# Kernel optimization log

Hardware: AMD Instinct MI355X
Metric: run time of the kernel (lower is better)

The kernel has to match this reference:

```python
import jax, jax.numpy as jnp
import numpy as np

N_NODES = 100000
N_EDGES = 800000
H_DIM = 128
E_DIM = 32
N_LAYER = 3


def setup_inputs() -> dict:
    key = jax.random.key(0)
    ks = jax.random.split(key, 5)
    x = jax.random.normal(ks[0], (N_NODES, H_DIM), dtype=jnp.float32)
    edge_index = jax.random.randint(ks[1], (2, N_EDGES), 0, N_NODES, dtype=jnp.int64)
    edge_attr = jax.random.normal(ks[2], (N_EDGES, E_DIM), dtype=jnp.float32)
    fan_in = 2 * H_DIM + E_DIM
    # torch Linear weight layout: [out_features, in_features]
    Wm = jax.random.normal(ks[3], (N_LAYER, H_DIM, fan_in), dtype=jnp.float32) / jnp.sqrt(fan_in)
    bm = jax.random.normal(ks[4], (N_LAYER, H_DIM), dtype=jnp.float32) * 0.01
    return {"x": x, "edge_index": edge_index, "edge_attr": edge_attr, "Wm": Wm, "bm": bm}


def reference(x, edge_index, edge_attr, Wm, bm):
    # PyG flow='source_to_target': row 0 = source (j), row 1 = target (i)
    src = edge_index[0]
    dst = edge_index[1]
    n_nodes = x.shape[0]
    n_layer = Wm.shape[0]
    for l in range(n_layer):  # small fixed layer count
        # message: m_ij = Linear(cat[x_j, x_i, edge_attr])
        m = jnp.concatenate([x[src], x[dst], edge_attr], axis=1)  # [E, 2h+e]
        m = jnp.einsum('ef,hf->eh', m, Wm[l]) + bm[l]             # [E, h]
        # aggr='add': scatter-add messages to target nodes
        x = jax.ops.segment_sum(m, dst, num_segments=n_nodes)     # [N, h]
        x = jax.nn.leaky_relu(x, negative_slope=0.01)
    # residual_connection='none' -> no-op; activate_last=True
    x = jax.nn.leaky_relu(x, negative_slope=0.01)
    return x
```

## Files before the change

### kernel.cpp

```cpp
#include <hip/hip_runtime.h>

#define N_NODES 100000
#define NP      100096
#define N_EDGES 800000
#define HD 128
#define ED 32
#define FAN 288
#define NL 3

#define SCHUNK 2048
#define SBLK   ((N_NODES + SCHUNK - 1) / SCHUNK)

typedef short bf16x8 __attribute__((ext_vector_type(8)));
typedef short bf16x4 __attribute__((ext_vector_type(4)));
typedef float f32x4  __attribute__((ext_vector_type(4)));

__device__ inline float b2f(short s) {
    unsigned u = ((unsigned)(unsigned short)s) << 16;
    return __builtin_bit_cast(float, u);
}
__device__ inline short f2b(float f) {
    unsigned u = __builtin_bit_cast(unsigned, f);
    unsigned r = u + 0x7FFFu + ((u >> 16) & 1u);
    return (short)(r >> 16);
}


__global__ void count_kernel(const int* __restrict__ dst, int* __restrict__ deg) {
    int e = blockIdx.x * 256 + threadIdx.x;
    if (e < N_EDGES) atomicAdd(&deg[dst[e]], 1);
}

__global__ void scan_reduce(const int* __restrict__ deg, int* __restrict__ bsum) {
    __shared__ int ws[4];
    const int tid = threadIdx.x;
    int i0 = blockIdx.x * SCHUNK + tid * 8;
    int t = 0;
    #pragma unroll
    for (int j = 0; j < 8; ++j) {
        int i = i0 + j;
        if (i < N_NODES) t += deg[i];
    }
    #pragma unroll
    for (int off = 32; off >= 1; off >>= 1) t += __shfl_down(t, off, 64);
    if ((tid & 63) == 0) ws[tid >> 6] = t;
    __syncthreads();
    if (tid == 0) bsum[blockIdx.x] = ws[0] + ws[1] + ws[2] + ws[3];
}

__global__ void scan_mid(const int* __restrict__ bsum, int* __restrict__ boff,
                         int* __restrict__ ptr) {
    int lane = threadIdx.x;
    int v = (lane < SBLK) ? bsum[lane] : 0;
    int s = v;
    #pragma unroll
    for (int off = 1; off < 64; off <<= 1) {
        int t = __shfl_up(s, off, 64);
        if (lane >= off) s += t;
    }
    if (lane < SBLK) boff[lane] = s - v;
    if (lane == 63) ptr[N_NODES] = s;
}

__global__ void scan_final(const int* __restrict__ deg, const int* __restrict__ boff,
                           int* __restrict__ ptr, int* __restrict__ cursor) {
    __shared__ int wsum[4];
    const int tid = threadIdx.x;
    const int lane = tid & 63, wid = tid >> 6;
    int i0 = blockIdx.x * SCHUNK + tid * 8;
    int v[8]; int tsum = 0;
    #pragma unroll
    for (int j = 0; j < 8; ++j) {
        int i = i0 + j;
        v[j] = (i < N_NODES) ? deg[i] : 0;
        tsum += v[j];
    }
    int s = tsum;
    #pragma unroll
    for (int off = 1; off < 64; off <<= 1) {
        int t = __shfl_up(s, off, 64);
        if (lane >= off) s += t;
    }
    if (lane == 63) wsum[wid] = s;
    __syncthreads();
    int woff = 0;
    #pragma unroll
    for (int w = 0; w < 4; ++w) if (w < wid) woff += wsum[w];
    int excl = boff[blockIdx.x] + woff + (s - tsum);
    #pragma unroll
    for (int j = 0; j < 8; ++j) {
        int i = i0 + j;
        if (i < N_NODES) { ptr[i] = excl; cursor[i] = excl; }
        excl += v[j];
    }
}

__global__ void fill_kernel(const int* __restrict__ src, const int* __restrict__ dst,
                            int* __restrict__ cursor, int2* __restrict__ csr2) {
    int e = blockIdx.x * 256 + threadIdx.x;
    if (e < N_EDGES) {
        int d = dst[e];
        int slot = atomicAdd(&cursor[d], 1);
        csr2[slot] = make_int2(src[e], e);
    }
}

__global__ void permute_eattr(const int2* __restrict__ csr2, const float* __restrict__ eattr,
                              short* __restrict__ ecsr) {
    int idx = blockIdx.x * 256 + threadIdx.x;
    int s = idx >> 3;
    int g = idx & 7;
    if (s >= N_EDGES) return;
    int e = csr2[s].y;
    float4 v = *reinterpret_cast<const float4*>(eattr + (size_t)e * ED + g * 4);
    bf16x4 o;
    o[0] = f2b(v.x); o[1] = f2b(v.y); o[2] = f2b(v.z); o[3] = f2b(v.w);
    *reinterpret_cast<bf16x4*>(ecsr + (size_t)s * ED + g * 4) = o;
}

__global__ void edge_sum(const short* __restrict__ ecsr, const int* __restrict__ ptr,
                         short* __restrict__ agge, float* __restrict__ degf) {
    int node = blockIdx.x * 32 + (threadIdx.x >> 3);
    int g = threadIdx.x & 7;
    if (node >= N_NODES) return;
    int s0 = ptr[node], s1 = ptr[node + 1];
    float a[4] = {};
    for (int s = s0; s < s1; ++s) {
        bf16x4 v = *reinterpret_cast<const bf16x4*>(ecsr + (size_t)s * ED + g * 4);
        #pragma unroll
        for (int j = 0; j < 4; ++j) a[j] += b2f(v[j]);
    }
    bf16x4 o;
    #pragma unroll
    for (int j = 0; j < 4; ++j) o[j] = f2b(a[j]);
    *reinterpret_cast<bf16x4*>(agge + (size_t)node * ED + g * 4) = o;
    if (g == 0) degf[node] = (float)(s1 - s0);
}

__global__ void wconv_kernel(const float* __restrict__ Wm, short* __restrict__ Wb) {
    int idx = blockIdx.x * 256 + threadIdx.x;
    if (idx < NL * HD * FAN) Wb[idx] = f2b(Wm[idx]);
}

__global__ void xconv_kernel(const float* __restrict__ x, const float* __restrict__ degf,
                             short* __restrict__ xb, short* __restrict__ xd) {
    int i4 = blockIdx.x * 256 + threadIdx.x;
    if (i4 >= N_NODES * (HD / 4)) return;
    int row = i4 >> 5;
    float d = degf[row];
    float4 v = reinterpret_cast<const float4*>(x)[i4];
    bf16x4 o, od;
    float vv[4] = {v.x, v.y, v.z, v.w};
    #pragma unroll
    for (int j = 0; j < 4; ++j) {
        short s = f2b(vv[j]);
        o[j] = s;
        od[j] = f2b(b2f(s) * d);
    }
    *reinterpret_cast<bf16x4*>(xb + (size_t)i4 * 4) = o;
    *reinterpret_cast<bf16x4*>(xd + (size_t)i4 * 4) = od;
}

__global__ void aggregate_kernel(const int* __restrict__ ptr, const int2* __restrict__ csr2,
                                 const short* __restrict__ x, short* __restrict__ agg) {
    int node = blockIdx.x * 16 + (threadIdx.x >> 4);
    int g = threadIdx.x & 15;
    if (node >= N_NODES) return;
    int s0 = ptr[node], s1 = ptr[node + 1];
    float acc0[8] = {}, acc1[8] = {};
    int s = s0;
    int i0 = (s < s1) ? csr2[s].x : 0;
    int i1 = (s + 1 < s1) ? csr2[s + 1].x : 0;
    for (; s + 2 <= s1;) {
        bf16x8 v0 = *reinterpret_cast<const bf16x8*>(x + (size_t)i0 * HD + g * 8);
        bf16x8 v1 = *reinterpret_cast<const bf16x8*>(x + (size_t)i1 * HD + g * 8);
        s += 2;
        i0 = (s < s1) ? csr2[s].x : 0;
        i1 = (s + 1 < s1) ? csr2[s + 1].x : 0;
        #pragma unroll
        for (int j = 0; j < 8; ++j) acc0[j] += b2f(v0[j]);
        #pragma unroll
        for (int j = 0; j < 8; ++j) acc1[j] += b2f(v1[j]);
    }
    if (s < s1) {
        bf16x8 v0 = *reinterpret_cast<const bf16x8*>(x + (size_t)i0 * HD + g * 8);
        #pragma unroll
        for (int j = 0; j < 8; ++j) acc0[j] += b2f(v0[j]);
    }
    bf16x8 o;
    #pragma unroll
    for (int j = 0; j < 8; ++j) o[j] = f2b(acc0[j] + acc1[j]);
    *reinterpret_cast<bf16x8*>(agg + (size_t)node * HD + g * 8) = o;
}

__global__ __launch_bounds__(256) void gemm_mfma(
    const short* __restrict__ aggs,
    const short* __restrict__ xdeg,
    const short* __restrict__ agge,
    const float* __restrict__ degf,
    const short* __restrict__ Wb,
    const float* __restrict__ b,
    float* __restrict__ out_f32,
    short* __restrict__ out_x,
    short* __restrict__ out_xd,
    int last)
{
    const int tid = threadIdx.x;
    const int w = tid >> 6, lane = tid & 63;
    const int wy = w >> 1, wx = w & 1;
    const int m0 = blockIdx.x * 128;
    const int l15 = lane & 15, lq = lane >> 4;
    const int kb = lq * 8;
    const size_t arow = (size_t)(m0 + wy * 64 + l15);

    f32x4 acc[4][4];
    #pragma unroll
    for (int i = 0; i < 4; ++i)
        #pragma unroll
        for (int j = 0; j < 4; ++j) acc[i][j] = (f32x4){0.f, 0.f, 0.f, 0.f};

    #pragma unroll
    for (int kt = 0; kt < 9; ++kt) {
        const short* abase;
        int ld, ko;
        if (kt < 4)      { abase = aggs; ld = HD; ko = kt * 32; }
        else if (kt < 8) { abase = xdeg; ld = HD; ko = kt * 32 - 128; }
        else             { abase = agge; ld = ED; ko = 0; }

        bf16x8 a[4], bf[4];
        #pragma unroll
        for (int mf = 0; mf < 4; ++mf)
            a[mf] = *reinterpret_cast<const bf16x8*>(
                abase + (arow + (size_t)mf * 16) * ld + ko + kb);
        #pragma unroll
        for (int nf = 0; nf < 4; ++nf) {
            int c = wx * 64 + nf * 16 + l15;
            bf[nf] = *reinterpret_cast<const bf16x8*>(
                Wb + (size_t)c * FAN + kt * 32 + kb);
        }
        #pragma unroll
        for (int mf = 0; mf < 4; ++mf)
            #pragma unroll
            for (int nf = 0; nf < 4; ++nf)
                acc[mf][nf] = __builtin_amdgcn_mfma_f32_16x16x32_bf16(
                    a[mf], bf[nf], acc[mf][nf], 0, 0, 0);
    }

    #pragma unroll
    for (int mf = 0; mf < 4; ++mf) {
        int r0 = m0 + wy * 64 + mf * 16 + lq * 4;
        float dg[4];
        #pragma unroll
        for (int j = 0; j < 4; ++j)
            dg[j] = (r0 + j < N_NODES) ? degf[r0 + j] : 0.f;
        #pragma unroll
        for (int nf = 0; nf < 4; ++nf) {
            int c = wx * 64 + nf * 16 + l15;
            float bc = b[c];
            #pragma unroll
            for (int j = 0; j < 4; ++j) {
                int row = r0 + j;
                if (row >= N_NODES) continue;
                float v = acc[mf][nf][j] + dg[j] * bc;
                v = (v >= 0.f) ? v : 0.01f * v;
                if (last) {
                    v = (v >= 0.f) ? v : 0.01f * v;
                    out_f32[(size_t)row * HD + c] = v;
                } else {
                    short xb = f2b(v);
                    out_x[(size_t)row * HD + c] = xb;
                    out_xd[(size_t)row * HD + c] = f2b(b2f(xb) * dg[j]);
                }
            }
        }
    }
}

extern "C" void kernel_launch(void* const* d_in, const int* in_sizes, int n_in,
                              void* d_out, int out_size, void* d_ws, size_t ws_size,
                              hipStream_t stream) {
    const float* x_in  = (const float*)d_in[0];
    const int*   ei    = (const int*)d_in[1];
    const float* eattr = (const float*)d_in[2];
    const float* Wm    = (const float*)d_in[3];
    const float* bm    = (const float*)d_in[4];
    float* out = (float*)d_out;

    char* ws = (char*)d_ws;
    size_t off = 0;
    auto alloc = [&](size_t bytes) -> void* {
        void* p = ws + off;
        off = (off + bytes + 255) & ~(size_t)255;
        return p;
    };
    short* x_bf   = (short*)alloc((size_t)NP * HD * 2);
    short* xdeg   = (short*)alloc((size_t)NP * HD * 2);
    short* aggs   = (short*)alloc((size_t)NP * HD * 2);
    short* agge   = (short*)alloc((size_t)NP * ED * 2);
    float* degf   = (float*)alloc((size_t)NP * 4);
    int*   deg    = (int*)alloc((size_t)N_NODES * 4);
    int*   ptr    = (int*)alloc((size_t)(N_NODES + 1) * 4);
    int*   cursor = (int*)alloc((size_t)N_NODES * 4);
    int2*  csr2   = (int2*)alloc((size_t)N_EDGES * 8);
    short* Wb     = (short*)alloc((size_t)NL * HD * FAN * 2);
    int*   bsum   = (int*)alloc((size_t)SBLK * 4);
    int*   boff   = (int*)alloc((size_t)SBLK * 4);

    short* ecsr = x_bf;

    const int* src = ei;
    const int* dst = ei + N_EDGES;

    hipMemsetAsync(deg, 0, (size_t)N_NODES * 4, stream);
    count_kernel<<<(N_EDGES + 255) / 256, 256, 0, stream>>>(dst, deg);
    scan_reduce<<<SBLK, 256, 0, stream>>>(deg, bsum);
    scan_mid<<<1, 64, 0, stream>>>(bsum, boff, ptr);
    scan_final<<<SBLK, 256, 0, stream>>>(deg, boff, ptr, cursor);
    fill_kernel<<<(N_EDGES + 255) / 256, 256, 0, stream>>>(src, dst, cursor, csr2);
    permute_eattr<<<(N_EDGES * 8 + 255) / 256, 256, 0, stream>>>(csr2, eattr, ecsr);
    edge_sum<<<(N_NODES + 31) / 32, 256, 0, stream>>>(ecsr, ptr, agge, degf);
    wconv_kernel<<<(NL * HD * FAN + 255) / 256, 256, 0, stream>>>(Wm, Wb);
    xconv_kernel<<<(N_NODES * (HD / 4) + 255) / 256, 256, 0, stream>>>(x_in, degf, x_bf, xdeg);

    for (int l = 0; l < NL; ++l) {
        aggregate_kernel<<<(N_NODES + 15) / 16, 256, 0, stream>>>(ptr, csr2, x_bf, aggs);
        gemm_mfma<<<NP / 128, 256, 0, stream>>>(
            aggs, xdeg, agge, degf,
            Wb + (size_t)l * HD * FAN, bm + (size_t)l * HD,
            out, x_bf, xdeg, (l == NL - 1) ? 1 : 0);
    }
}
```

Baseline: 422.9 us.

## Fuse neighbor aggregation into the MFMA GEMM with ping-pong node buffers

```diff
diff --git a/kernel.cpp b/kernel.cpp
--- a/kernel.cpp
+++ b/kernel.cpp
@@ -161,40 +161,11 @@
     *reinterpret_cast<bf16x4*>(xd + (size_t)i4 * 4) = od;
 }
 
-__global__ void aggregate_kernel(const int* __restrict__ ptr, const int2* __restrict__ csr2,
-                                 const short* __restrict__ x, short* __restrict__ agg) {
-    int node = blockIdx.x * 16 + (threadIdx.x >> 4);
-    int g = threadIdx.x & 15;
-    if (node >= N_NODES) return;
-    int s0 = ptr[node], s1 = ptr[node + 1];
-    float acc0[8] = {}, acc1[8] = {};
-    int s = s0;
-    int i0 = (s < s1) ? csr2[s].x : 0;
-    int i1 = (s + 1 < s1) ? csr2[s + 1].x : 0;
-    for (; s + 2 <= s1;) {
-        bf16x8 v0 = *reinterpret_cast<const bf16x8*>(x + (size_t)i0 * HD + g * 8);
-        bf16x8 v1 = *reinterpret_cast<const bf16x8*>(x + (size_t)i1 * HD + g * 8);
-        s += 2;
-        i0 = (s < s1) ? csr2[s].x : 0;
-        i1 = (s + 1 < s1) ? csr2[s + 1].x : 0;
-        #pragma unroll
-        for (int j = 0; j < 8; ++j) acc0[j] += b2f(v0[j]);
-        #pragma unroll
-        for (int j = 0; j < 8; ++j) acc1[j] += b2f(v1[j]);
-    }
-    if (s < s1) {
-        bf16x8 v0 = *reinterpret_cast<const bf16x8*>(x + (size_t)i0 * HD + g * 8);
-        #pragma unroll
-        for (int j = 0; j < 8; ++j) acc0[j] += b2f(v0[j]);
-    }
-    bf16x8 o;
-    #pragma unroll
-    for (int j = 0; j < 8; ++j) o[j] = f2b(acc0[j] + acc1[j]);
-    *reinterpret_cast<bf16x8*>(agg + (size_t)node * HD + g * 8) = o;
-}
-
-__global__ __launch_bounds__(256) void gemm_mfma(
-    const short* __restrict__ aggs,
+#define TM 64
+
+__global__ __launch_bounds__(256) void fused_layer(
+    const int* __restrict__ ptr, const int2* __restrict__ csr2,
+    const short* __restrict__ xprev,
     const short* __restrict__ xdeg,
     const short* __restrict__ agge,
     const float* __restrict__ degf,
@@ -205,50 +176,108 @@
     short* __restrict__ out_xd,
     int last)
 {
+    __shared__ char As[TM * 256];
     const int tid = threadIdx.x;
+    const int m0 = blockIdx.x * TM;
+
+    {
+        const int ng = tid >> 4, g = tid & 15;
+        #pragma unroll
+        for (int i = 0; i < 4; ++i) {
+            int row = i * 16 + ng;
+            int node = m0 + row;
+            float acc0[8] = {}, acc1[8] = {};
+            if (node < N_NODES) {
+                int s0 = ptr[node], s1 = ptr[node + 1];
+                int s = s0;
+                int i0 = (s < s1) ? csr2[s].x : 0;
+                int i1 = (s + 1 < s1) ? csr2[s + 1].x : 0;
+                for (; s + 2 <= s1;) {
+                    bf16x8 v0 = *reinterpret_cast<const bf16x8*>(xprev + (size_t)i0 * HD + g * 8);
+                    bf16x8 v1 = *reinterpret_cast<const bf16x8*>(xprev + (size_t)i1 * HD + g * 8);
+                    s += 2;
+                    i0 = (s < s1) ? csr2[s].x : 0;
+                    i1 = (s + 1 < s1) ? csr2[s + 1].x : 0;
+                    #pragma unroll
+                    for (int j = 0; j < 8; ++j) acc0[j] += b2f(v0[j]);
+                    #pragma unroll
+                    for (int j = 0; j < 8; ++j) acc1[j] += b2f(v1[j]);
+                }
+                if (s < s1) {
+                    bf16x8 v0 = *reinterpret_cast<const bf16x8*>(xprev + (size_t)i0 * HD + g * 8);
+                    #pragma unroll
+                    for (int j = 0; j < 8; ++j) acc0[j] += b2f(v0[j]);
+                }
+            }
+            bf16x8 o;
+            #pragma unroll
+            for (int j = 0; j < 8; ++j) o[j] = f2b(acc0[j] + acc1[j]);
+            int byte = row * 256 + g * 16;
+            byte ^= (row & 7) << 4;
+            *reinterpret_cast<bf16x8*>(As + byte) = o;
+        }
+    }
+    __syncthreads();
+
     const int w = tid >> 6, lane = tid & 63;
     const int wy = w >> 1, wx = w & 1;
-    const int m0 = blockIdx.x * 128;
     const int l15 = lane & 15, lq = lane >> 4;
     const int kb = lq * 8;
-    const size_t arow = (size_t)(m0 + wy * 64 + l15);
-
-    f32x4 acc[4][4];
-    #pragma unroll
-    for (int i = 0; i < 4; ++i)
+
+    f32x4 acc[2][4];
+    #pragma unroll
+    for (int i = 0; i < 2; ++i)
         #pragma unroll
         for (int j = 0; j < 4; ++j) acc[i][j] = (f32x4){0.f, 0.f, 0.f, 0.f};
 
     #pragma unroll
-    for (int kt = 0; kt < 9; ++kt) {
-        const short* abase;
-        int ld, ko;
-        if (kt < 4)      { abase = aggs; ld = HD; ko = kt * 32; }
-        else if (kt < 8) { abase = xdeg; ld = HD; ko = kt * 32 - 128; }
-        else             { abase = agge; ld = ED; ko = 0; }
-
-        bf16x8 a[4], bf[4];
-        #pragma unroll
-        for (int mf = 0; mf < 4; ++mf)
-            a[mf] = *reinterpret_cast<const bf16x8*>(
-                abase + (arow + (size_t)mf * 16) * ld + ko + kb);
+    for (int kt = 0; kt < 4; ++kt) {
+        bf16x8 a[2], bf[4];
+        #pragma unroll
+        for (int mf = 0; mf < 2; ++mf) {
+            int row = wy * 32 + mf * 16 + l15;
+            int byte = row * 256 + kt * 64 + kb * 2;
+            byte ^= (row & 7) << 4;
+            a[mf] = *reinterpret_cast<const bf16x8*>(As + byte);
+        }
         #pragma unroll
         for (int nf = 0; nf < 4; ++nf) {
             int c = wx * 64 + nf * 16 + l15;
-            bf[nf] = *reinterpret_cast<const bf16x8*>(
-                Wb + (size_t)c * FAN + kt * 32 + kb);
-        }
-        #pragma unroll
-        for (int mf = 0; mf < 4; ++mf)
+            bf[nf] = *reinterpret_cast<const bf16x8*>(Wb + (size_t)c * FAN + kt * 32 + kb);
+        }
+        #pragma unroll
+        for (int mf = 0; mf < 2; ++mf)
             #pragma unroll
             for (int nf = 0; nf < 4; ++nf)
                 acc[mf][nf] = __builtin_amdgcn_mfma_f32_16x16x32_bf16(
                     a[mf], bf[nf], acc[mf][nf], 0, 0, 0);
     }
-
-    #pragma unroll
-    for (int mf = 0; mf < 4; ++mf) {
-        int r0 = m0 + wy * 64 + mf * 16 + lq * 4;
+    #pragma unroll
+    for (int kt = 4; kt < 9; ++kt) {
+        bf16x8 a[2], bf[4];
+        #pragma unroll
+        for (int mf = 0; mf < 2; ++mf) {
+            size_t arow = (size_t)(m0 + wy * 32 + mf * 16 + l15);
+            a[mf] = (kt < 8)
+                ? *reinterpret_cast<const bf16x8*>(xdeg + arow * HD + (kt * 32 - 128) + kb)
+                : *reinterpret_cast<const bf16x8*>(agge + arow * ED + kb);
+        }
+        #pragma unroll
+        for (int nf = 0; nf < 4; ++nf) {
+            int c = wx * 64 + nf * 16 + l15;
+            bf[nf] = *reinterpret_cast<const bf16x8*>(Wb + (size_t)c * FAN + kt * 32 + kb);
+        }
+        #pragma unroll
+        for (int mf = 0; mf < 2; ++mf)
+            #pragma unroll
+            for (int nf = 0; nf < 4; ++nf)
+                acc[mf][nf] = __builtin_amdgcn_mfma_f32_16x16x32_bf16(
+                    a[mf], bf[nf], acc[mf][nf], 0, 0, 0);
+    }
+
+    #pragma unroll
+    for (int mf = 0; mf < 2; ++mf) {
+        int r0 = m0 + wy * 32 + mf * 16 + lq * 4;
         float dg[4];
         #pragma unroll
         for (int j = 0; j < 4; ++j)
@@ -293,9 +322,9 @@
         off = (off + bytes + 255) & ~(size_t)255;
         return p;
     };
-    short* x_bf   = (short*)alloc((size_t)NP * HD * 2);
+    short* x0     = (short*)alloc((size_t)NP * HD * 2);
+    short* x1     = (short*)alloc((size_t)NP * HD * 2);
     short* xdeg   = (short*)alloc((size_t)NP * HD * 2);
-    short* aggs   = (short*)alloc((size_t)NP * HD * 2);
     short* agge   = (short*)alloc((size_t)NP * ED * 2);
     float* degf   = (float*)alloc((size_t)NP * 4);
     int*   deg    = (int*)alloc((size_t)N_NODES * 4);
@@ -306,7 +335,7 @@
     int*   bsum   = (int*)alloc((size_t)SBLK * 4);
     int*   boff   = (int*)alloc((size_t)SBLK * 4);
 
-    short* ecsr = x_bf;
+    short* ecsr = x0;
 
     const int* src = ei;
     const int* dst = ei + N_EDGES;
@@ -320,13 +349,13 @@
     permute_eattr<<<(N_EDGES * 8 + 255) / 256, 256, 0, stream>>>(csr2, eattr, ecsr);
     edge_sum<<<(N_NODES + 31) / 32, 256, 0, stream>>>(ecsr, ptr, agge, degf);
     wconv_kernel<<<(NL * HD * FAN + 255) / 256, 256, 0, stream>>>(Wm, Wb);
-    xconv_kernel<<<(N_NODES * (HD / 4) + 255) / 256, 256, 0, stream>>>(x_in, degf, x_bf, xdeg);
-
+    xconv_kernel<<<(N_NODES * (HD / 4) + 255) / 256, 256, 0, stream>>>(x_in, degf, x0, xdeg);
+
+    short* xping[2] = {x0, x1};
     for (int l = 0; l < NL; ++l) {
-        aggregate_kernel<<<(N_NODES + 15) / 16, 256, 0, stream>>>(ptr, csr2, x_bf, aggs);
-        gemm_mfma<<<NP / 128, 256, 0, stream>>>(
-            aggs, xdeg, agge, degf,
+        fused_layer<<<NP / TM, 256, 0, stream>>>(
+            ptr, csr2, xping[l & 1], xdeg, agge, degf,
             Wb + (size_t)l * HD * FAN, bm + (size_t)l * HD,
-            out, x_bf, xdeg, (l == NL - 1) ? 1 : 0);
-    }
-}
+            out, xping[(l + 1) & 1], xdeg, (l == NL - 1) ? 1 : 0);
+    }
+}
```

Result: faster. 372.9 us (-11.8%).
